# Kernel tuning notes

Measured on AMD Instinct MI355X. Metric: run time of the kernel, lower is better.

## Reference

```python
import jax, jax.numpy as jnp
import numpy as np
from itertools import permutations, combinations

NB_OBJ = 5
DIM_BODY = 10
DIM_OBJ = 15
N_PERM = NB_OBJ * (NB_OBJ - 1)      # 20 edges
HID = 256                            # MLP hidden size
DMP = 128                            # dim_mp_output
ACT = 4                              # action dim
BATCH = 32768
GOAL_DIM = 30                        # 10 close + 20 above predicates
LOG_STD_MIN, LOG_STD_MAX = -20.0, 2.0


def _graph_tables():
    combos = list(combinations(range(NB_OBJ), 2))   # 10 unordered pairs
    perms = list(permutations(range(NB_OBJ), 2))    # 20 ordered pairs
    edges = np.array(perms, dtype=np.int32)          # [20, 2]
    pred = []
    for k, (i, j) in enumerate(perms):
        close_id = combos.index(tuple(sorted((i, j))))
        above_ij = 10 + k
        above_ji = 10 + perms.index((j, i))
        pred.append([close_id, above_ij, above_ji])
    return edges, np.array(pred, dtype=np.int32)     # [20,2], [20,3]


def _linear_params(key, fan_in, fan_out):
    kw, kb = jax.random.split(key)
    scale = 1.0 / np.sqrt(fan_in)
    W = jax.random.uniform(kw, (fan_in, fan_out), jnp.float32, -scale, scale)
    b = jax.random.uniform(kb, (fan_out,), jnp.float32, -scale, scale)
    return W, b


def setup_inputs() -> dict:
    key = jax.random.key(0)
    ks = jax.random.split(key, 16)
    edges, pred_ids = _graph_tables()
    dim_mp_in = DIM_BODY + 3 + 3 + 3   # 19
    W1, b1 = _linear_params(ks[0], dim_mp_in, HID)
    W2, b2 = _linear_params(ks[1], HID, DMP)
    Wq, bq = _linear_params(ks[2], DMP, DMP)
    Wk, bk = _linear_params(ks[3], DMP, DMP)
    Wv, bv = _linear_params(ks[4], DMP, DMP)
    Wr, br = _linear_params(ks[5], DMP, HID)
    Wm, bm = _linear_params(ks[6], HID, ACT)
    Ws, bs = _linear_params(ks[7], HID, ACT)
    obs = jax.random.normal(ks[8], (BATCH, DIM_BODY + NB_OBJ * DIM_OBJ), jnp.float32)
    ag = jax.random.uniform(ks[9], (BATCH, GOAL_DIM), jnp.float32)
    g = jax.random.uniform(ks[10], (BATCH, GOAL_DIM), jnp.float32)
    return {
        "obs": obs, "ag": ag, "g": g,
        "W1": W1, "b1": b1, "W2": W2, "b2": b2,
        "Wq": Wq, "bq": bq, "Wk": Wk, "bk": bk, "Wv": Wv, "bv": bv,
        "Wr": Wr, "br": br, "Wm": Wm, "bm": bm, "Ws": Ws, "bs": bs,
        "edges": jnp.asarray(edges), "pred_ids": jnp.asarray(pred_ids),
    }


def reference(obs, ag, g, W1, b1, W2, b2, Wq, bq, Wk, bk, Wv, bv,
              Wr, br, Wm, bm, Ws, bs, edges, pred_ids):
    B = obs.shape[0]
    obs_body = obs[:, :DIM_BODY]                                   # [B, 10]
    obs_objects = obs[:, DIM_BODY:].reshape(B, NB_OBJ, DIM_OBJ)    # [B, 5, 15]
    delta_g = g - ag                                               # [B, 30]

    # Vectorized edge-feature gather (original loops over 20 permutations).
    body = jnp.broadcast_to(obs_body[None], (N_PERM, B, DIM_BODY))         # [P,B,10]
    dg = delta_g[:, pred_ids].transpose(1, 0, 2)                           # [P,B,3]
    src = obs_objects[:, edges[:, 0], :3].transpose(1, 0, 2)               # [P,B,3]
    tgt = obs_objects[:, edges[:, 1], :3].transpose(1, 0, 2)               # [P,B,3]
    inp_mp = jnp.concatenate([body, dg, src, tgt], axis=-1)                # [P,B,19]

    # GnnMessagePassing: 2-layer ReLU MLP
    h = jax.nn.relu(inp_mp @ W1 + b1)                                      # [P,B,256]
    edge_feat = jax.nn.relu(h @ W2 + b2)                                   # [P,B,128]
    x = edge_feat.transpose(1, 0, 2)                                       # [B,P,128]

    # SelfAttention over the 20 edges (single head, scaled dot product)
    q = x @ Wq + bq
    k = x @ Wk + bk
    v = x @ Wv + bv
    scores = jnp.einsum('bpd,bqd->bpq', q, k) / jnp.sqrt(jnp.float32(DMP))  # [B,P,P]
    attn = jax.nn.softmax(scores, axis=-1)
    x = jnp.einsum('bpq,bqd->bpd', attn, v)                                 # [B,P,128]

    pooled = x.sum(axis=-2)                                                 # [B,128]

    # RhoActorDeepSet
    hr = jax.nn.relu(pooled @ Wr + br)                                      # [B,256]
    mean = hr @ Wm + bm                                                     # [B,4]
    log_std = jnp.clip(hr @ Ws + bs, LOG_STD_MIN, LOG_STD_MAX)              # [B,4]
    return (mean, log_std)
```

## Files before the change

kernel.cpp:

```cpp
#include <hip/hip_runtime.h>
#include <hip/hip_bf16.h>

#define NB_OBJ   5
#define DIM_BODY 10
#define DIM_OBJ  15
#define N_PERM   20
#define HID      256
#define DMP      128
#define ACT      4
#define BATCH    32768
#define GOAL_DIM 30
#define DIN      19
#define OBS_LEN  85
#define TB       4
#define MROWS    80

typedef __hip_bfloat16 bf16;
typedef __attribute__((ext_vector_type(8))) short s16x8;
typedef __attribute__((ext_vector_type(4))) float f32x4;
typedef __attribute__((ext_vector_type(2))) unsigned u32x2;

#define MFMA16(a, b, c) __builtin_amdgcn_mfma_f32_16x16x32_bf16((a), (b), (c), 0, 0, 0)

#define OFF_W1   0
#define OFF_W2   8192
#define OFF_M    40960
#define OFF_WV   57344
#define OFF_WR   73728
#define OFF_WP   106496
#define PACK_TOTAL 106624

__device__ __forceinline__ unsigned short bfr(float x) {
    return (unsigned short)((__float_as_uint(x) + 0x8000u) >> 16);
}
__device__ __forceinline__ unsigned pkbf(float a, float b) {
    return ((__float_as_uint(a) + 0x8000u) >> 16)
         | ((__float_as_uint(b) + 0x8000u) & 0xffff0000u);
}

__device__ __forceinline__ s16x8 frag_lds(const bf16* base, int m, int stride, int kof, int bprm) {
    int phys = (((kof >> 3) ^ (m & bprm)) << 3);
    return *(const s16x8*)(base + m * stride + phys);
}

__device__ __forceinline__ void store_c4(bf16* base, int m, int stride, int n0,
                                         int bprm, f32x4 acc, f32x4 bs, bool do_relu) {
    float v0 = acc[0] + bs[0], v1 = acc[1] + bs[1];
    float v2 = acc[2] + bs[2], v3 = acc[3] + bs[3];
    if (do_relu) {
        v0 = fmaxf(v0, 0.f); v1 = fmaxf(v1, 0.f);
        v2 = fmaxf(v2, 0.f); v3 = fmaxf(v3, 0.f);
    }
    u32x2 w;
    w.x = pkbf(v0, v1);
    w.y = pkbf(v2, v3);
    int blk = ((n0 >> 3) ^ (m & bprm));
    *(u32x2*)(base + m * stride + blk * 8 + (n0 & 7)) = w;
}

__device__ __forceinline__ void pack_tiled(const float* __restrict__ W, int Kact, int N,
                                           int KT, bf16* __restrict__ dst, int idx) {
    int tile = idx >> 9;
    int r    = idx & 511;
    int kt   = tile % KT, nt = tile / KT;
    int c    = r >> 7;
    int rem  = r & 127;
    int n16  = rem >> 3, j = rem & 7;
    int k    = kt * 32 + c * 8 + j;
    float v  = (k < Kact) ? W[k * N + nt * 16 + n16] : 0.f;
    dst[idx] = __float2bfloat16(v);
}

__global__ __launch_bounds__(256) void prepack_kernel(
    const float* __restrict__ W1, const float* __restrict__ b1,
    const float* __restrict__ W2,
    const float* __restrict__ Wq, const float* __restrict__ bq,
    const float* __restrict__ Wk,
    const float* __restrict__ Wv, const float* __restrict__ Wr,
    bf16* __restrict__ ws) {
    const float scl = 0.08838834764831845f;
    int idx = blockIdx.x * 256 + threadIdx.x;
    if (idx < 8192) {
        int nt = idx >> 9, r = idx & 511;
        int c = r >> 7, rem = r & 127, n16 = rem >> 3, j = rem & 7;
        int k = c * 8 + j, n = nt * 16 + n16;
        float v = (k < DIN) ? W1[k * HID + n] : (k == DIN ? b1[n] : 0.f);
        ws[OFF_W1 + idx] = __float2bfloat16(v);
    }
    else if (idx < 40960) pack_tiled(W2, 256, 128, 8, ws + OFF_W2, idx - 8192);
    else if (idx < 57344) {
        int i2 = idx - 40960;
        int tile = i2 >> 9, r = i2 & 511;
        int kt = tile & 3, nt = tile >> 2;
        int c = r >> 7, rem = r & 127, n16 = rem >> 3, j = rem & 7;
        int d = kt * 32 + c * 8 + j;
        int e = nt * 16 + n16;
        float s = 0.f;
        for (int j2 = 0; j2 < DMP; ++j2) s += Wq[d * DMP + j2] * Wk[e * DMP + j2];
        ws[OFF_M + i2] = __float2bfloat16(s * scl);
    }
    else if (idx < 73728)  pack_tiled(Wv, 128, 128, 4, ws + OFF_WV, idx - 57344);
    else if (idx < 106496) pack_tiled(Wr, 128, 256, 4, ws + OFF_WR, idx - 73728);
    else if (idx < PACK_TOTAL) {
        int d = idx - OFF_WP;
        float s = 0.f;
        for (int j2 = 0; j2 < DMP; ++j2) s += Wk[d * DMP + j2] * bq[j2];
        ((float*)(ws + OFF_WP))[d] = s * scl;
    }
}

__global__ __launch_bounds__(256, 3) void actor_main(
    const float* __restrict__ obs, const float* __restrict__ ag, const float* __restrict__ g,
    const float* __restrict__ b2v, const float* __restrict__ bvv, const float* __restrict__ brv,
    const float* __restrict__ Wm, const float* __restrict__ bm,
    const float* __restrict__ Wsc, const float* __restrict__ bsv,
    const int* __restrict__ edges, const int* __restrict__ pred_ids,
    const bf16* __restrict__ wp, float* __restrict__ out)
{
    const int b0   = blockIdx.x * TB;
    const int tid  = threadIdx.x;
    const int lane = tid & 63;
    const int wav  = tid >> 6;
    const int l15  = lane & 15;
    const int lq   = lane >> 4;

    __shared__ __align__(16) union {
        struct {
            float obs_[TB][OBS_LEN];
            float dg[TB][GOAL_DIM];
            int   edg[N_PERM * 2];
            int   prd[N_PERM * 3];
            bf16  inp[MROWS][40];
        } a;
        struct {
            float sc[TB][N_PERM][N_PERM];
            float cs[TB][N_PERM];
            bf16  y[TB][DMP];
            bf16  pooled[16][DMP];
        } p;
    } rA;
    __shared__ __align__(16) union {
        bf16 hall[MROWS][DMP];
        bf16 t[MROWS][DMP];
    } rB;
    __shared__ __align__(16) union {
        bf16 x[MROWS][DMP];
        struct { float hr[TB][HID]; float red[32][9]; } h;
    } rC;

    const f32x4 zf = {0.f, 0.f, 0.f, 0.f};

    for (int i = tid; i < TB * OBS_LEN; i += 256)
        ((float*)rA.a.obs_)[i] = obs[b0 * OBS_LEN + i];
    if (tid < TB * GOAL_DIM) ((float*)rA.a.dg)[tid] = g[b0 * GOAL_DIM + tid] - ag[b0 * GOAL_DIM + tid];
    if (tid < N_PERM * 2)    rA.a.edg[tid] = edges[tid];
    if (tid < N_PERM * 3)    rA.a.prd[tid] = pred_ids[tid];
    __syncthreads();

    for (int idx = tid; idx < MROWS * 32; idx += 256) {
        int m = idx >> 5, c = idx & 31;
        int bi = m / N_PERM, p = m - bi * N_PERM;
        float v = 0.f;
        if      (c < 10) v = rA.a.obs_[bi][c];
        else if (c < 13) v = rA.a.dg[bi][rA.a.prd[p * 3 + (c - 10)]];
        else if (c < 16) v = rA.a.obs_[bi][DIM_BODY + rA.a.edg[p * 2 + 0] * DIM_OBJ + (c - 13)];
        else if (c < 19) v = rA.a.obs_[bi][DIM_BODY + rA.a.edg[p * 2 + 1] * DIM_OBJ + (c - 16)];
        else if (c == 19) v = 1.0f;
        *(unsigned short*)&rA.a.inp[m][c] = bfr(v);
    }
    __syncthreads();

    s16x8 xfr[5];
    #pragma unroll
    for (int mt = 0; mt < 5; ++mt)
        xfr[mt] = *(const s16x8*)(&rA.a.inp[mt * 16 + l15][lq * 8]);

    f32x4 m2a[5], m2b[5];
    #pragma unroll
    for (int mt = 0; mt < 5; ++mt) { m2a[mt] = zf; m2b[mt] = zf; }
    const int nt0 = wav * 2, nt1 = nt0 + 1;

    #pragma unroll
    for (int ph = 0; ph < 2; ++ph) {
        #pragma unroll
        for (int ntl = 0; ntl < 2; ++ntl) {
            int ntg = ph * 8 + wav * 2 + ntl;
            s16x8 wfr = *(const s16x8*)(wp + OFF_W1 + ntg * 512 + (lq * 16 + l15) * 8);
            int nloc = (wav * 2 + ntl) * 16 + lq * 4;
            #pragma unroll
            for (int mt = 0; mt < 5; ++mt) {
                f32x4 acc = MFMA16(wfr, xfr[mt], zf);
                store_c4(&rB.hall[0][0], mt * 16 + l15, DMP, nloc, 15, acc, zf, true);
            }
        }
        __syncthreads();
        #pragma unroll
        for (int ktl = 0; ktl < 4; ++ktl) {
            int ktg = ph * 4 + ktl;
            s16x8 wf0 = *(const s16x8*)(wp + OFF_W2 + (nt0 * 8 + ktg) * 512 + (lq * 16 + l15) * 8);
            s16x8 wf1 = *(const s16x8*)(wp + OFF_W2 + (nt1 * 8 + ktg) * 512 + (lq * 16 + l15) * 8);
            #pragma unroll
            for (int mt = 0; mt < 5; ++mt) {
                s16x8 a = frag_lds(&rB.hall[0][0], mt * 16 + l15, DMP, ktl * 32 + lq * 8, 15);
                m2a[mt] = MFMA16(wf0, a, m2a[mt]);
                m2b[mt] = MFMA16(wf1, a, m2b[mt]);
            }
        }
        __syncthreads();
    }
    {
        f32x4 bs0 = *(const f32x4*)(b2v + nt0 * 16 + lq * 4);
        f32x4 bs1 = *(const f32x4*)(b2v + nt1 * 16 + lq * 4);
        #pragma unroll
        for (int mt = 0; mt < 5; ++mt) {
            int m = mt * 16 + l15;
            store_c4(&rC.x[0][0], m, DMP, nt0 * 16 + lq * 4, 15, m2a[mt], bs0, true);
            store_c4(&rC.x[0][0], m, DMP, nt1 * 16 + lq * 4, 15, m2b[mt], bs1, true);
        }
    }
    __syncthreads();

    {
        const float* wf = (const float*)(wp + OFF_WP);
        f32x4 a0[5], a1[5];
        #pragma unroll
        for (int mt = 0; mt < 5; ++mt) { a0[mt] = zf; a1[mt] = zf; }
        #pragma unroll
        for (int kt = 0; kt < 4; ++kt) {
            s16x8 wf0 = *(const s16x8*)(wp + OFF_M + (nt0 * 4 + kt) * 512 + (lq * 16 + l15) * 8);
            s16x8 wf1 = *(const s16x8*)(wp + OFF_M + (nt1 * 4 + kt) * 512 + (lq * 16 + l15) * 8);
            #pragma unroll
            for (int mt = 0; mt < 5; ++mt) {
                s16x8 a = frag_lds(&rC.x[0][0], mt * 16 + l15, DMP, kt * 32 + lq * 8, 15);
                a0[mt] = MFMA16(wf0, a, a0[mt]);
                a1[mt] = MFMA16(wf1, a, a1[mt]);
            }
        }
        f32x4 bs0 = *(const f32x4*)(wf + nt0 * 16 + lq * 4);
        f32x4 bs1 = *(const f32x4*)(wf + nt1 * 16 + lq * 4);
        #pragma unroll
        for (int mt = 0; mt < 5; ++mt) {
            int m = mt * 16 + l15;
            store_c4(&rB.t[0][0], m, DMP, nt0 * 16 + lq * 4, 15, a0[mt], bs0, false);
            store_c4(&rB.t[0][0], m, DMP, nt1 * 16 + lq * 4, 15, a1[mt], bs1, false);
        }
    }
    __syncthreads();

    {
        const int bi = wav;
        const int r0 = bi * N_PERM;
        f32x4 c00 = zf, c01 = zf, c10 = zf, c11 = zf;
        #pragma unroll
        for (int kt = 0; kt < 4; ++kt) {
            int kof = kt * 32 + lq * 8;
            s16x8 a0 = frag_lds(&rB.t[0][0], r0 + l15,      DMP, kof, 15);
            s16x8 a1 = frag_lds(&rB.t[0][0], r0 + 16 + l15, DMP, kof, 15);
            s16x8 k0 = frag_lds(&rC.x[0][0], r0 + l15,      DMP, kof, 15);
            s16x8 k1 = frag_lds(&rC.x[0][0], r0 + 16 + l15, DMP, kof, 15);
            c00 = MFMA16(a0, k0, c00);  c01 = MFMA16(a0, k1, c01);
            c10 = MFMA16(a1, k0, c10);  c11 = MFMA16(a1, k1, c11);
        }
        #pragma unroll
        for (int r = 0; r < 4; ++r) {
            int pr = lq * 4 + r, qc = l15;
            rA.p.sc[bi][pr][qc] = c00[r];
            if (qc + 16 < N_PERM) rA.p.sc[bi][pr][qc + 16] = c01[r];
            if (pr + 16 < N_PERM) {
                rA.p.sc[bi][pr + 16][qc] = c10[r];
                if (qc + 16 < N_PERM) rA.p.sc[bi][pr + 16][qc + 16] = c11[r];
            }
        }
    }

    if (lane < N_PERM) {
        float* scrow = rA.p.sc[wav][lane];
        float mx = -1e30f;
        #pragma unroll
        for (int qq = 0; qq < N_PERM; ++qq) mx = fmaxf(mx, scrow[qq]);
        float sum = 0.f;
        #pragma unroll
        for (int qq = 0; qq < N_PERM; ++qq) { float e = __expf(scrow[qq] - mx); scrow[qq] = e; sum += e; }
        float inv = 1.f / sum;
        #pragma unroll
        for (int qq = 0; qq < N_PERM; ++qq) scrow[qq] *= inv;
    }
    if (lane < N_PERM) {
        float cs = 0.f;
        #pragma unroll
        for (int p = 0; p < N_PERM; ++p) cs += rA.p.sc[wav][p][lane];
        rA.p.cs[wav][lane] = cs;
    }

    {
        int bi = wav, j0 = lane * 2;
        float a0 = 0.f, a1 = 0.f;
        #pragma unroll
        for (int qq = 0; qq < N_PERM; ++qq) {
            int row  = bi * N_PERM + qq;
            int vcol = ((((j0 >> 3) ^ (row & 15)) << 3) | (j0 & 7));
            unsigned w = *(const unsigned*)(&rC.x[row][vcol]);
            float c = rA.p.cs[bi][qq];
            a0 += c * __uint_as_float(w << 16);
            a1 += c * __uint_as_float(w & 0xffff0000u);
        }
        int pcol = ((((j0 >> 3) ^ (bi & 15)) << 3) | (j0 & 7));
        *(unsigned*)(&rA.p.y[bi][pcol]) = pkbf(a0, a1);
    }
    __syncthreads();

    {
        s16x8 pfr[4];
        #pragma unroll
        for (int kt = 0; kt < 4; ++kt)
            pfr[kt] = frag_lds(&rA.p.y[0][0], l15, DMP, kt * 32 + lq * 8, 15);
        f32x4 acc0 = zf, acc1 = zf;
        #pragma unroll
        for (int kt = 0; kt < 4; ++kt) {
            s16x8 wf0 = *(const s16x8*)(wp + OFF_WV + (nt0 * 4 + kt) * 512 + (lq * 16 + l15) * 8);
            s16x8 wf1 = *(const s16x8*)(wp + OFF_WV + (nt1 * 4 + kt) * 512 + (lq * 16 + l15) * 8);
            acc0 = MFMA16(wf0, pfr[kt], acc0);
            acc1 = MFMA16(wf1, pfr[kt], acc1);
        }
        f32x4 bs0 = *(const f32x4*)(bvv + nt0 * 16 + lq * 4);
        f32x4 bs1 = *(const f32x4*)(bvv + nt1 * 16 + lq * 4);
        #pragma unroll
        for (int r = 0; r < 4; ++r) { bs0[r] *= 20.f; bs1[r] *= 20.f; }
        store_c4(&rA.p.pooled[0][0], l15, DMP, nt0 * 16 + lq * 4, 15, acc0, bs0, false);
        store_c4(&rA.p.pooled[0][0], l15, DMP, nt1 * 16 + lq * 4, 15, acc1, bs1, false);
    }
    __syncthreads();

    {
        s16x8 pfr[4];
        #pragma unroll
        for (int kt = 0; kt < 4; ++kt)
            pfr[kt] = frag_lds(&rA.p.pooled[0][0], l15, DMP, kt * 32 + lq * 8, 15);
        f32x4 acc[4];
        #pragma unroll
        for (int i = 0; i < 4; ++i) acc[i] = zf;
        #pragma unroll
        for (int kt = 0; kt < 4; ++kt)
            #pragma unroll
            for (int i = 0; i < 4; ++i) {
                int nt = wav * 4 + i;
                s16x8 wf = *(const s16x8*)(wp + OFF_WR + (nt * 4 + kt) * 512 + (lq * 16 + l15) * 8);
                acc[i] = MFMA16(wf, pfr[kt], acc[i]);
            }
        if (l15 < TB) {
            #pragma unroll
            for (int i = 0; i < 4; ++i) {
                int n0 = (wav * 4 + i) * 16 + lq * 4;
                f32x4 bs = *(const f32x4*)(brv + n0);
                f32x4 o;
                #pragma unroll
                for (int r = 0; r < 4; ++r) o[r] = fmaxf(acc[i][r] + bs[r], 0.f);
                *(f32x4*)(&rC.h.hr[l15][n0]) = o;
            }
        }
    }
    __syncthreads();

    {
        int o = tid & 31, cch = tid >> 5;
        int bi = o >> 3, rr = o & 7;
        bool is_mean = rr < ACT;
        int a = rr & (ACT - 1);
        const float* W = is_mean ? Wm : Wsc;
        float part = 0.f;
        int k0 = cch * 32;
        #pragma unroll 8
        for (int kk = k0; kk < k0 + 32; ++kk) part += rC.h.hr[bi][kk] * W[kk * ACT + a];
        rC.h.red[o][cch] = part;
    }
    __syncthreads();
    if (tid < 32) {
        int bi = tid >> 3, rr = tid & 7;
        bool is_mean = rr < ACT;
        int a = rr & (ACT - 1);
        float acc = is_mean ? bm[a] : bsv[a];
        #pragma unroll
        for (int c = 0; c < 8; ++c) acc += rC.h.red[tid][c];
        if (!is_mean) acc = fminf(fmaxf(acc, -20.f), 2.f);
        out[(is_mean ? 0 : BATCH * ACT) + (b0 + bi) * ACT + a] = acc;
    }
}

extern "C" void kernel_launch(void* const* d_in, const int* in_sizes, int n_in,
                              void* d_out, int out_size, void* d_ws, size_t ws_size,
                              hipStream_t stream) {
    (void)in_sizes; (void)n_in; (void)out_size; (void)ws_size;
    const float* obs = (const float*)d_in[0];
    const float* ag  = (const float*)d_in[1];
    const float* g   = (const float*)d_in[2];
    const float* W1  = (const float*)d_in[3];
    const float* b1  = (const float*)d_in[4];
    const float* W2  = (const float*)d_in[5];
    const float* b2  = (const float*)d_in[6];
    const float* Wq  = (const float*)d_in[7];
    const float* bq  = (const float*)d_in[8];
    const float* Wk  = (const float*)d_in[9];
    const float* Wv  = (const float*)d_in[11];
    const float* bv  = (const float*)d_in[12];
    const float* Wr  = (const float*)d_in[13];
    const float* br  = (const float*)d_in[14];
    const float* Wm  = (const float*)d_in[15];
    const float* bm  = (const float*)d_in[16];
    const float* Ws  = (const float*)d_in[17];
    const float* bs  = (const float*)d_in[18];
    const int*  edges    = (const int*)d_in[19];
    const int*  pred_ids = (const int*)d_in[20];
    float* out = (float*)d_out;
    bf16*  wp  = (bf16*)d_ws;

    prepack_kernel<<<(PACK_TOTAL + 255) / 256, 256, 0, stream>>>(
        W1, b1, W2, Wq, bq, Wk, Wv, Wr, wp);
    actor_main<<<BATCH / TB, 256, 0, stream>>>(
        obs, ag, g, b2, bv, br, Wm, bm, Ws, bs,
        edges, pred_ids, wp, out);
}
```

Baseline: 277.7 us.

## Use MFMA for output heads, precomputed gather table, vectorize prepack dot products

Replaces the scalar two-stage reduction for the mean/log_std heads with a single-wave MFMA over a packed bf16 head weight, storing hr in bf16 LDS. Input assembly now uses a prepacked index table into a flat per-sample buffer, so the per-element branches on edges and predicate ids go away. Prepack dot products for the folded Q·K matrix are vectorized with float4 loads. The bf16 hidden activations and head weights add rounding error to the outputs.

```diff
diff --git a/kernel.cpp b/kernel.cpp
--- a/kernel.cpp
+++ b/kernel.cpp
@@ -28,7 +28,9 @@
 #define OFF_WV   57344
 #define OFF_WR   73728
 #define OFF_WP   106496
-#define PACK_TOTAL 106624
+#define OFF_WH   106752
+#define OFF_TBL  110848
+#define PACK_TOTAL 111360
 
 __device__ __forceinline__ unsigned short bfr(float x) {
     return (unsigned short)((__float_as_uint(x) + 0x8000u) >> 16);
@@ -77,6 +79,8 @@
     const float* __restrict__ Wq, const float* __restrict__ bq,
     const float* __restrict__ Wk,
     const float* __restrict__ Wv, const float* __restrict__ Wr,
+    const float* __restrict__ Wm, const float* __restrict__ Wsc,
+    const int* __restrict__ edges, const int* __restrict__ pred_ids,
     bf16* __restrict__ ws) {
     const float scl = 0.08838834764831845f;
     int idx = blockIdx.x * 256 + threadIdx.x;
@@ -95,26 +99,57 @@
         int c = r >> 7, rem = r & 127, n16 = rem >> 3, j = rem & 7;
         int d = kt * 32 + c * 8 + j;
         int e = nt * 16 + n16;
+        const float4* qr = (const float4*)(Wq + d * DMP);
+        const float4* kr = (const float4*)(Wk + e * DMP);
         float s = 0.f;
-        for (int j2 = 0; j2 < DMP; ++j2) s += Wq[d * DMP + j2] * Wk[e * DMP + j2];
+        #pragma unroll 8
+        for (int t = 0; t < 32; ++t) {
+            float4 a = qr[t], b = kr[t];
+            s += a.x * b.x + a.y * b.y + a.z * b.z + a.w * b.w;
+        }
         ws[OFF_M + i2] = __float2bfloat16(s * scl);
     }
     else if (idx < 73728)  pack_tiled(Wv, 128, 128, 4, ws + OFF_WV, idx - 57344);
     else if (idx < 106496) pack_tiled(Wr, 128, 256, 4, ws + OFF_WR, idx - 73728);
+    else if (idx < 106624) {
+        int d = idx - 106496;
+        const float4* kr = (const float4*)(Wk + d * DMP);
+        const float4* bq4 = (const float4*)bq;
+        float s = 0.f;
+        #pragma unroll 8
+        for (int t = 0; t < 32; ++t) {
+            float4 a = kr[t], b = bq4[t];
+            s += a.x * b.x + a.y * b.y + a.z * b.z + a.w * b.w;
+        }
+        ((float*)(ws + OFF_WP))[d] = s * scl;
+    }
+    else if (idx < 110720) {
+        int i2 = idx - 106624;
+        int kt = i2 >> 9, r = i2 & 511;
+        int c = r >> 7, rem = r & 127, o = rem >> 3, j = rem & 7;
+        int k = kt * 32 + c * 8 + j;
+        float v = (o < ACT) ? Wm[k * ACT + o]
+                : (o < 2 * ACT) ? Wsc[k * ACT + (o - ACT)] : 0.f;
+        ws[OFF_WH + i2] = __float2bfloat16(v);
+    }
     else if (idx < PACK_TOTAL) {
-        int d = idx - OFF_WP;
-        float s = 0.f;
-        for (int j2 = 0; j2 < DMP; ++j2) s += Wk[d * DMP + j2] * bq[j2];
-        ((float*)(ws + OFF_WP))[d] = s * scl;
+        int i2 = idx - 110720;
+        int p = i2 >> 5, c = i2 & 31;
+        short t;
+        if      (c < 10) t = (short)c;
+        else if (c < 13) t = (short)(OBS_LEN + pred_ids[p * 3 + (c - 10)]);
+        else if (c < 16) t = (short)(DIM_BODY + edges[p * 2 + 0] * DIM_OBJ + (c - 13));
+        else if (c < 19) t = (short)(DIM_BODY + edges[p * 2 + 1] * DIM_OBJ + (c - 16));
+        else if (c == 19) t = 115;
+        else              t = 116;
+        ((short*)(ws + OFF_TBL))[i2] = t;
     }
 }
 
 __global__ __launch_bounds__(256, 3) void actor_main(
     const float* __restrict__ obs, const float* __restrict__ ag, const float* __restrict__ g,
     const float* __restrict__ b2v, const float* __restrict__ bvv, const float* __restrict__ brv,
-    const float* __restrict__ Wm, const float* __restrict__ bm,
-    const float* __restrict__ Wsc, const float* __restrict__ bsv,
-    const int* __restrict__ edges, const int* __restrict__ pred_ids,
+    const float* __restrict__ bm, const float* __restrict__ bsv,
     const bf16* __restrict__ wp, float* __restrict__ out)
 {
     const int b0   = blockIdx.x * TB;
@@ -126,10 +161,8 @@
 
     __shared__ __align__(16) union {
         struct {
-            float obs_[TB][OBS_LEN];
-            float dg[TB][GOAL_DIM];
-            int   edg[N_PERM * 2];
-            int   prd[N_PERM * 3];
+            float flat[TB][120];
+            short tbl[N_PERM * 32];
             bf16  inp[MROWS][40];
         } a;
         struct {
@@ -145,27 +178,28 @@
     } rB;
     __shared__ __align__(16) union {
         bf16 x[MROWS][DMP];
-        struct { float hr[TB][HID]; float red[32][9]; } h;
+        bf16 hr[16][HID];
     } rC;
 
     const f32x4 zf = {0.f, 0.f, 0.f, 0.f};
 
-    for (int i = tid; i < TB * OBS_LEN; i += 256)
-        ((float*)rA.a.obs_)[i] = obs[b0 * OBS_LEN + i];
-    if (tid < TB * GOAL_DIM) ((float*)rA.a.dg)[tid] = g[b0 * GOAL_DIM + tid] - ag[b0 * GOAL_DIM + tid];
-    if (tid < N_PERM * 2)    rA.a.edg[tid] = edges[tid];
-    if (tid < N_PERM * 3)    rA.a.prd[tid] = pred_ids[tid];
+    for (int i = tid; i < TB * 120; i += 256) {
+        int bi = i / 120, c = i - bi * 120;
+        float v = 0.f;
+        if      (c < OBS_LEN) v = obs[(b0 + bi) * OBS_LEN + c];
+        else if (c < 115)     v = g[(b0 + bi) * GOAL_DIM + (c - OBS_LEN)]
+                                - ag[(b0 + bi) * GOAL_DIM + (c - OBS_LEN)];
+        else if (c == 115)    v = 1.0f;
+        rA.a.flat[bi][c] = v;
+    }
+    for (int i = tid; i < N_PERM * 32; i += 256)
+        ((short*)rA.a.tbl)[i] = ((const short*)(wp + OFF_TBL))[i];
     __syncthreads();
 
     for (int idx = tid; idx < MROWS * 32; idx += 256) {
         int m = idx >> 5, c = idx & 31;
         int bi = m / N_PERM, p = m - bi * N_PERM;
-        float v = 0.f;
-        if      (c < 10) v = rA.a.obs_[bi][c];
-        else if (c < 13) v = rA.a.dg[bi][rA.a.prd[p * 3 + (c - 10)]];
-        else if (c < 16) v = rA.a.obs_[bi][DIM_BODY + rA.a.edg[p * 2 + 0] * DIM_OBJ + (c - 13)];
-        else if (c < 19) v = rA.a.obs_[bi][DIM_BODY + rA.a.edg[p * 2 + 1] * DIM_OBJ + (c - 16)];
-        else if (c == 19) v = 1.0f;
+        float v = rA.a.flat[bi][rA.a.tbl[p * 32 + c]];
         *(unsigned short*)&rA.a.inp[m][c] = bfr(v);
     }
     __syncthreads();
@@ -347,42 +381,37 @@
                 s16x8 wf = *(const s16x8*)(wp + OFF_WR + (nt * 4 + kt) * 512 + (lq * 16 + l15) * 8);
                 acc[i] = MFMA16(wf, pfr[kt], acc[i]);
             }
-        if (l15 < TB) {
-            #pragma unroll
-            for (int i = 0; i < 4; ++i) {
-                int n0 = (wav * 4 + i) * 16 + lq * 4;
-                f32x4 bs = *(const f32x4*)(brv + n0);
-                f32x4 o;
+        #pragma unroll
+        for (int i = 0; i < 4; ++i) {
+            int n0 = (wav * 4 + i) * 16 + lq * 4;
+            f32x4 bs = *(const f32x4*)(brv + n0);
+            store_c4(&rC.hr[0][0], l15, HID, n0, 15, acc[i], bs, true);
+        }
+    }
+    __syncthreads();
+
+    if (wav == 0) {
+        f32x4 acc = zf;
+        #pragma unroll
+        for (int kt = 0; kt < 8; ++kt) {
+            s16x8 wh = *(const s16x8*)(wp + OFF_WH + kt * 512 + (lq * 16 + l15) * 8);
+            s16x8 hf = frag_lds(&rC.hr[0][0], l15, HID, kt * 32 + lq * 8, 15);
+            acc = MFMA16(wh, hf, acc);
+        }
+        if (l15 < TB && lq < 2) {
+            int bi = l15;
+            if (lq == 0) {
                 #pragma unroll
-                for (int r = 0; r < 4; ++r) o[r] = fmaxf(acc[i][r] + bs[r], 0.f);
-                *(f32x4*)(&rC.h.hr[l15][n0]) = o;
-            }
-        }
-    }
-    __syncthreads();
-
-    {
-        int o = tid & 31, cch = tid >> 5;
-        int bi = o >> 3, rr = o & 7;
-        bool is_mean = rr < ACT;
-        int a = rr & (ACT - 1);
-        const float* W = is_mean ? Wm : Wsc;
-        float part = 0.f;
-        int k0 = cch * 32;
-        #pragma unroll 8
-        for (int kk = k0; kk < k0 + 32; ++kk) part += rC.h.hr[bi][kk] * W[kk * ACT + a];
-        rC.h.red[o][cch] = part;
-    }
-    __syncthreads();
-    if (tid < 32) {
-        int bi = tid >> 3, rr = tid & 7;
-        bool is_mean = rr < ACT;
-        int a = rr & (ACT - 1);
-        float acc = is_mean ? bm[a] : bsv[a];
-        #pragma unroll
-        for (int c = 0; c < 8; ++c) acc += rC.h.red[tid][c];
-        if (!is_mean) acc = fminf(fmaxf(acc, -20.f), 2.f);
-        out[(is_mean ? 0 : BATCH * ACT) + (b0 + bi) * ACT + a] = acc;
+                for (int r = 0; r < 4; ++r)
+                    out[(b0 + bi) * ACT + r] = acc[r] + bm[r];
+            } else {
+                #pragma unroll
+                for (int r = 0; r < 4; ++r) {
+                    float v = acc[r] + bsv[r];
+                    out[BATCH * ACT + (b0 + bi) * ACT + r] = fminf(fmaxf(v, -20.f), 2.f);
+                }
+            }
+        }
     }
 }
 
@@ -414,8 +443,7 @@
     bf16*  wp  = (bf16*)d_ws;
 
     prepack_kernel<<<(PACK_TOTAL + 255) / 256, 256, 0, stream>>>(
-        W1, b1, W2, Wq, bq, Wk, Wv, Wr, wp);
+        W1, b1, W2, Wq, bq, Wk, Wv, Wr, Wm, Ws, edges, pred_ids, wp);
     actor_main<<<BATCH / TB, 256, 0, stream>>>(
-        obs, ag, g, b2, bv, br, Wm, bm, Ws, bs,
-        edges, pred_ids, wp, out);
-}
+        obs, ag, g, b2, bv, br, bm, bs, wp, out);
+}
```

Result: faster. 252.9 us (-8.9%).
